# Optimization experiments

Measured on AMD Instinct MI355X. Metric: run time of the kernel, lower is better.

The kernel has to match this reference:

```python
import jax, jax.numpy as jnp
import numpy as np

N_QUBITS = 12
N_LAYERS = 4
BATCH = 1024


def _apply_1q(state, U, wire):
    # state: (B,) + (2,)*N complex; U: (2,2) shared or (B,2,2) batched.
    x = jnp.moveaxis(state, 1 + wire, 1)
    if U.ndim == 3:
        x = jnp.einsum('bij,bj...->bi...', U, x)
    else:
        x = jnp.einsum('ij,bj...->bi...', U, x)
    return jnp.moveaxis(x, 1, 1 + wire)


def _apply_cnot(state, c, t):
    # CNOT: flip target axis on the control=1 slice.
    x = jnp.moveaxis(state, (1 + c, 1 + t), (1, 2))
    x = x.at[:, 1].set(x[:, 1, ::-1])
    return jnp.moveaxis(x, (1, 2), (1 + c, 1 + t))


def _rot_matrices(w):
    # PennyLane Rot(phi, theta, omega) = RZ(omega) RY(theta) RZ(phi); w: (N, 3) -> (N, 2, 2)
    phi, theta, omega = w[:, 0], w[:, 1], w[:, 2]
    c = jnp.cos(theta / 2).astype(jnp.complex64)
    s = jnp.sin(theta / 2).astype(jnp.complex64)
    ep = jnp.exp(0.5j * (phi + omega).astype(jnp.complex64))  # e^{+i(phi+omega)/2}
    em = jnp.exp(0.5j * (phi - omega).astype(jnp.complex64))  # e^{+i(phi-omega)/2}
    m00 = jnp.conj(ep) * c
    m01 = -em * s
    m10 = jnp.conj(em) * s
    m11 = ep * c
    return jnp.stack([jnp.stack([m00, m01], -1), jnp.stack([m10, m11], -1)], -2)


def _circuit(x, weights):
    B = x.shape[0]
    n = N_QUBITS
    # |0...0> initial state, batched, shaped (B, 2, 2, ..., 2)
    state = jnp.zeros((B, 2 ** n), jnp.complex64).at[:, 0].set(1.0)
    state = state.reshape((B,) + (2,) * n)
    # Angle encoding: RY(pi * x_i) on wire i (batched gate matrices)
    half = jnp.pi * x / 2  # (B, n)
    c = jnp.cos(half).astype(jnp.complex64)
    s = jnp.sin(half).astype(jnp.complex64)
    ry = jnp.stack([jnp.stack([c, -s], -1), jnp.stack([s, c], -1)], -2)  # (B, n, 2, 2)
    for i in range(n):
        state = _apply_1q(state, ry[:, i], i)
    # CNOT ring
    for i in range(n):
        state = _apply_cnot(state, i, (i + 1) % n)
    # StronglyEntanglingLayers, default ranges r_l = (l % (n-1)) + 1
    for l in range(N_LAYERS):
        U = _rot_matrices(weights[l])
        for i in range(n):
            state = _apply_1q(state, U[i], i)
        r = l % (n - 1) + 1
        for i in range(n):
            state = _apply_cnot(state, i, (i + r) % n)
    # PauliZ expectations: <Z_i> = sum_k |psi_k|^2 * (-1)^{bit_i(k)}
    probs = (state.real ** 2 + state.imag ** 2).reshape(B, 2 ** n)
    ks = np.arange(2 ** n)
    bits = (ks[:, None] >> (n - 1 - np.arange(n))) & 1  # wire 0 = most significant axis
    signs = jnp.asarray(1.0 - 2.0 * bits, jnp.float32)  # (2^n, n)
    return probs @ signs  # (B, n)


def setup_inputs():
    key = jax.random.key(0)
    k1, k2 = jax.random.split(key)
    x = jax.random.uniform(k1, (BATCH, N_QUBITS), jnp.float32)
    weights = jax.random.uniform(k2, (N_LAYERS, N_QUBITS, 3), jnp.float32)
    return {"x": x, "weights": weights}


def reference(x, weights):
    return _circuit(x, weights)
```

## Files before the change

kernel.cpp:

```cpp
#include <hip/hip_runtime.h>

#define NQ 12
#define NLAYERS 4

typedef float v2f __attribute__((ext_vector_type(2)));
typedef unsigned uint2v __attribute__((ext_vector_type(2)));

template<int CTRL>
__device__ __forceinline__ float dppmov(float v) {
    return __uint_as_float((unsigned)__builtin_amdgcn_update_dpp(
        0, (int)__float_as_uint(v), CTRL, 0xF, 0xF, true));
}

template<int LB>
__device__ __forceinline__ float lx(float v, int lane) {
    if constexpr (LB == 0) {
        return dppmov<0xB1>(v);
    } else if constexpr (LB == 1) {
        return dppmov<0x4E>(v);
    } else if constexpr (LB == 2) {
        float a = dppmov<0x124>(v);
        float b = dppmov<0x12C>(v);
        return (lane & 4) ? a : b;
    } else if constexpr (LB == 3) {
        return dppmov<0x128>(v);
    } else if constexpr (LB == 4) {
#if __has_builtin(__builtin_amdgcn_permlane16_swap)
        uint2v r = __builtin_amdgcn_permlane16_swap(__float_as_uint(v), __float_as_uint(v), false, false);
        return __uint_as_float(r.x) + __uint_as_float(r.y) - v;
#else
        return __shfl_xor(v, 16, 64);
#endif
    } else {
#if __has_builtin(__builtin_amdgcn_permlane32_swap)
        uint2v r = __builtin_amdgcn_permlane32_swap(__float_as_uint(v), __float_as_uint(v), false, false);
        return __uint_as_float(r.x) + __uint_as_float(r.y) - v;
#else
        return __shfl_xor(v, 32, 64);
#endif
    }
}

template<int LB>
__device__ __forceinline__ v2f lxv(v2f a, int lane) {
    v2f r;
    r.x = lx<LB>(a.x, lane);
    r.y = lx<LB>(a.y, lane);
    return r;
}

__device__ __forceinline__ v2f swap2(v2f a) { return __builtin_shufflevector(a, a, 1, 0); }

template<int S>
__host__ __device__ constexpr int ringsrc_c(int k) {
    int s = k;
    for (int i = 11; i >= 0; --i) {
        const int pc = 11 - i;
        const int pt = 11 - ((i + S) % 12);
        s ^= ((s >> pc) & 1) << pt;
    }
    return s;
}

__host__ __device__ constexpr int ror1_4(int m) {
    return ((m >> 1) | ((m & 1) << 3)) & 15;
}
__host__ __device__ constexpr int phys_lin(int s) {
    return s ^ ror1_4((s >> 4) & 15);
}

struct LUT16 { int v[16]; };

template<int S>
__host__ __device__ constexpr LUT16 make_lr() {
    LUT16 a{};
    for (int r = 0; r < 16; ++r) a.v[r] = ringsrc_c<S>(r);
    return a;
}
template<int S>
__host__ __device__ constexpr LUT16 make_pr() {
    LUT16 a{};
    for (int r = 0; r < 16; ++r) a.v[r] = phys_lin(ringsrc_c<S>(r));
    return a;
}

template<int S>
__host__ __device__ constexpr bool grp_used(int h) {
    for (int r = 0; r < 16; ++r)
        if (((ringsrc_c<S>(r) >> 10) & 3) == h) return true;
    return false;
}


template<int RB>
__device__ __forceinline__ void gate_reg(v2f (&st)[16], const v2f* __restrict__ M) {
    const v2f m00xx = M[0], m00yy = M[1], m01xx = M[2], m01yy = M[3];
    const v2f m10xx = M[4], m10yy = M[5], m11xx = M[6], m11yy = M[7];
    #pragma unroll
    for (int r = 0; r < 16; ++r) if (!(r & (1 << RB))) {
        const int r1 = r | (1 << RB);
        v2f a0 = st[r], a1 = st[r1];
        st[r]  = m00xx * a0 + m00yy * swap2(a0) + m01xx * a1 + m01yy * swap2(a1);
        st[r1] = m10xx * a0 + m10yy * swap2(a0) + m11xx * a1 + m11yy * swap2(a1);
    }
}

template<int LB>
__device__ __forceinline__ void gate_lane(v2f (&st)[16], int lane, const v2f* __restrict__ M) {
    const bool hi = (lane >> LB) & 1;
    const v2f mSxx = hi ? M[6] : M[0], mSyy = hi ? M[7] : M[1];
    const v2f mOxx = hi ? M[4] : M[2], mOyy = hi ? M[5] : M[3];
    #pragma unroll
    for (int r = 0; r < 16; ++r) {
        v2f own = st[r];
        v2f oth = lxv<LB>(own, lane);
        st[r] = mSxx * own + mSyy * swap2(own) + mOxx * oth + mOyy * swap2(oth);
    }
}

template<int S, int H>
__device__ __forceinline__ void trip_group(v2f (&st)[16], int pb, int rowbase,
                                           const v2f* xch, const v2f* m4) {
    if constexpr (grp_used<S>(H)) {
        const int row = rowbase ^ H;
        v2f mxx[4], myy[4];
        #pragma unroll
        for (int j = 0; j < 4; ++j) {
            mxx[j] = m4[(row * 4 + j) * 2 + 0];
            myy[j] = m4[(row * 4 + j) * 2 + 1];
        }
        constexpr LUT16 LR = make_lr<S>();
        constexpr LUT16 PR = make_pr<S>();
        #pragma unroll
        for (int r = 0; r < 16; ++r) {
            if (((LR.v[r] >> 10) & 3) == H) {
                const int a = (pb ^ PR.v[r]) & 1023;
                v2f o0 = xch[a];
                v2f o1 = xch[a + 1024];
                v2f o2 = xch[a + 2048];
                v2f o3 = xch[a + 3072];
                st[r] = mxx[0] * o0 + myy[0] * swap2(o0)
                      + mxx[1] * o1 + myy[1] * swap2(o1)
                      + mxx[2] * o2 + myy[2] * swap2(o2)
                      + mxx[3] * o3 + myy[3] * swap2(o3);
            }
        }
    }
}

template<int S>
__device__ __forceinline__ void fused_trip(v2f (&st)[16], int wbase, int lsw,
                                           v2f* xch, const v2f* m4) {
    #pragma unroll
    for (int r = 0; r < 16; ++r) xch[wbase | (r ^ lsw)] = st[r];
    __syncthreads();
    const int sb = ringsrc_c<S>(wbase);
    const int pb = phys_lin(sb);
    const int rowbase = (sb >> 10) & 3;
    trip_group<S, 0>(st, pb, rowbase, xch, m4);
    trip_group<S, 1>(st, pb, rowbase, xch, m4);
    trip_group<S, 2>(st, pb, rowbase, xch, m4);
    trip_group<S, 3>(st, pb, rowbase, xch, m4);
    __syncthreads();
}

template<int S>
__device__ __forceinline__ void do_layer(v2f (&st)[16], int lane, int wbase, int lsw,
                                         v2f* xch, const v2f* m4,
                                         const v2f* __restrict__ Mw) {
    gate_lane<5>(st, lane, Mw + 2 * 8);
    gate_lane<4>(st, lane, Mw + 3 * 8);
    gate_lane<3>(st, lane, Mw + 4 * 8);
    gate_lane<2>(st, lane, Mw + 5 * 8);
    gate_lane<1>(st, lane, Mw + 6 * 8);
    gate_lane<0>(st, lane, Mw + 7 * 8);
    gate_reg<3>(st, Mw + 8 * 8);
    gate_reg<2>(st, Mw + 9 * 8);
    gate_reg<1>(st, Mw + 10 * 8);
    gate_reg<0>(st, Mw + 11 * 8);
    fused_trip<S>(st, wbase, lsw, xch, m4);
}

__global__ void prep_mats(const float* __restrict__ w3, v2f* __restrict__ mats) {
    int t = threadIdx.x;
    if (t < NLAYERS * NQ) {
        float phi = w3[t * 3 + 0], th = w3[t * 3 + 1], om = w3[t * 3 + 2];
        float ct = cosf(0.5f * th), s = sinf(0.5f * th);
        float ap = 0.5f * (phi + om), am = 0.5f * (phi - om);
        float cap = cosf(ap), sap = sinf(ap);
        float cam = cosf(am), sam = sinf(am);
        float2 m00 = make_float2( cap * ct, -sap * ct);
        float2 m01 = make_float2(-cam * s,  -sam * s);
        float2 m10 = make_float2( cam * s,  -sam * s);
        float2 m11 = make_float2( cap * ct,  sap * ct);
        v2f* M = mats + t * 8;
        M[0] = v2f{m00.x, m00.x};  M[1] = v2f{-m00.y, m00.y};
        M[2] = v2f{m01.x, m01.x};  M[3] = v2f{-m01.y, m01.y};
        M[4] = v2f{m10.x, m10.x};  M[5] = v2f{-m10.y, m10.y};
        M[6] = v2f{m11.x, m11.x};  M[7] = v2f{-m11.y, m11.y};
    }
    if (t < NLAYERS) {
        const int l = t;
        float2 mm[2][2][2];
        for (int w = 0; w < 2; ++w) {
            float phi = w3[(l * NQ + w) * 3 + 0], th = w3[(l * NQ + w) * 3 + 1],
                  om  = w3[(l * NQ + w) * 3 + 2];
            float ct = cosf(0.5f * th), s = sinf(0.5f * th);
            float ap = 0.5f * (phi + om), am = 0.5f * (phi - om);
            float cap = cosf(ap), sap = sinf(ap);
            float cam = cosf(am), sam = sinf(am);
            mm[w][0][0] = make_float2( cap * ct, -sap * ct);
            mm[w][0][1] = make_float2(-cam * s,  -sam * s);
            mm[w][1][0] = make_float2( cam * s,  -sam * s);
            mm[w][1][1] = make_float2( cap * ct,  sap * ct);
        }
        v2f* M4 = mats + NLAYERS * 96 + l * 32;
        for (int i = 0; i < 4; ++i)
            for (int j = 0; j < 4; ++j) {
                float2 a = mm[0][i >> 1][j >> 1];
                float2 bq = mm[1][i & 1][j & 1];
                float2 pq = make_float2(a.x * bq.x - a.y * bq.y, a.x * bq.y + a.y * bq.x);
                M4[(i * 4 + j) * 2 + 0] = v2f{pq.x, pq.x};
                M4[(i * 4 + j) * 2 + 1] = v2f{-pq.y, pq.y};
            }
    }
}

__device__ __forceinline__ float wsum(float v, int lane) {
    v += lx<5>(v, lane); v += lx<4>(v, lane); v += lx<3>(v, lane);
    v += lx<2>(v, lane); v += lx<1>(v, lane); v += lx<0>(v, lane);
    return v;
}

__global__ __launch_bounds__(256)
__attribute__((amdgpu_waves_per_eu(2, 4)))
void qsim_kernel(
    const float* __restrict__ x,
    const v2f* __restrict__ mats,
    float* __restrict__ out)
{
    __shared__ v2f xch[4096];
    __shared__ v2f m4l[NLAYERS * 32];

    const int b     = blockIdx.x;
    const int tid   = threadIdx.x;
    const int wv    = tid >> 6;
    const int lane  = tid & 63;
    const int wbase = (wv << 10) | (lane << 4);
    const int lsw   = ror1_4(lane & 15);

    if (tid < NLAYERS * 32) m4l[tid] = mats[NLAYERS * 96 + tid];

    const float PI = 3.14159265358979323846f;

    float cs[12], sn[12];
    #pragma unroll
    for (int w = 0; w < 12; ++w) {
        float h = 0.5f * PI * x[b * NQ + w];
        __sincosf(h, &sn[w], &cs[w]);
    }
    const int sbi = ringsrc_c<1>(wbase);
    float LF = 1.f;
    #pragma unroll
    for (int w = 2; w < 8; ++w)
        LF *= ((sbi >> (11 - w)) & 1) ? sn[w] : cs[w];
    constexpr LUT16 L1R = make_lr<1>();
    v2f st[16];
    #pragma unroll
    for (int r = 0; r < 16; ++r) {
        const int idx = sbi ^ L1R.v[r];
        float f = LF;
        f *= ((idx >> 11) & 1) ? sn[0]  : cs[0];
        f *= ((idx >> 10) & 1) ? sn[1]  : cs[1];
        f *= ((idx >> 3) & 1)  ? sn[8]  : cs[8];
        f *= ((idx >> 2) & 1)  ? sn[9]  : cs[9];
        f *= ((idx >> 1) & 1)  ? sn[10] : cs[10];
        f *= ( idx       & 1)  ? sn[11] : cs[11];
        st[r] = v2f{f, 0.f};
    }

    do_layer<1>(st, lane, wbase, lsw, xch, m4l + 0,   mats + 0);
    do_layer<2>(st, lane, wbase, lsw, xch, m4l + 32,  mats + 96);
    do_layer<3>(st, lane, wbase, lsw, xch, m4l + 64,  mats + 192);
    do_layer<4>(st, lane, wbase, lsw, xch, m4l + 96,  mats + 288);

    float S = 0.f;
    float aR[4] = {0.f, 0.f, 0.f, 0.f};
    #pragma unroll
    for (int r = 0; r < 16; ++r) {
        v2f sq = st[r] * st[r];
        float pr = sq.x + sq.y;
        S += pr;
        #pragma unroll
        for (int rb = 0; rb < 4; ++rb)
            aR[rb] += ((r >> rb) & 1) ? -pr : pr;
    }

    float* red = (float*)xch;

    {
        float T = wsum(S, lane);
        if (lane == 0) {
            red[wv * 12 + 0] = ((wv >> 1) & 1) ? -T : T;
            red[wv * 12 + 1] = (wv & 1) ? -T : T;
        }
    }
    #pragma unroll
    for (int W = 2; W < 8; ++W) {
        float v0 = ((lane >> (7 - W)) & 1) ? -S : S;
        v0 = wsum(v0, lane);
        if (lane == 0) red[wv * 12 + W] = v0;
    }
    #pragma unroll
    for (int W = 8; W < 12; ++W) {
        float v0 = wsum(aR[11 - W], lane);
        if (lane == 0) red[wv * 12 + W] = v0;
    }
    __syncthreads();
    if (tid < 12)
        out[b * NQ + tid] = red[tid] + red[12 + tid] + red[24 + tid] + red[36 + tid];
}

extern "C" void kernel_launch(void* const* d_in, const int* in_sizes, int n_in,
                              void* d_out, int out_size, void* d_ws, size_t ws_size,
                              hipStream_t stream) {
    const float* x  = (const float*)d_in[0];
    const float* w3 = (const float*)d_in[1];
    float* out = (float*)d_out;
    v2f* mats = (v2f*)d_ws;
    int batch = in_sizes[0] / NQ;
    prep_mats<<<1, 64, 0, stream>>>(w3, mats);
    qsim_kernel<<<batch, 256, 0, stream>>>(x, mats, out);
}
```

Measured before the change: 59.07 us.

## Process two batch items per block, interleaving gate compute with LDS exchange

Each block now simulates two batch elements, keeping two state register sets, and alternates so that the register-local gates of one state run while the other state's shared-memory exchange read is pending. The 4x4 exchange matrices are now read from global memory instead of being staged in LDS. The grid is halved and the waves_per_eu hint is relaxed. This aims to hide LDS latency and barrier stalls behind ALU work, at the cost of doubled register pressure, lower occupancy and more barriers per element pair.

```diff
diff --git a/kernel.cpp b/kernel.cpp
--- a/kernel.cpp
+++ b/kernel.cpp
@@ -83,7 +83,6 @@
     for (int r = 0; r < 16; ++r) a.v[r] = phys_lin(ringsrc_c<S>(r));
     return a;
 }
-
 template<int S>
 __host__ __device__ constexpr bool grp_used(int h) {
     for (int r = 0; r < 16; ++r)
@@ -118,16 +117,34 @@
     }
 }
 
+__device__ __forceinline__ void do_gates(v2f (&st)[16], int lane, const v2f* __restrict__ Mw) {
+    gate_lane<5>(st, lane, Mw + 2 * 8);
+    gate_lane<4>(st, lane, Mw + 3 * 8);
+    gate_lane<3>(st, lane, Mw + 4 * 8);
+    gate_lane<2>(st, lane, Mw + 5 * 8);
+    gate_lane<1>(st, lane, Mw + 6 * 8);
+    gate_lane<0>(st, lane, Mw + 7 * 8);
+    gate_reg<3>(st, Mw + 8 * 8);
+    gate_reg<2>(st, Mw + 9 * 8);
+    gate_reg<1>(st, Mw + 10 * 8);
+    gate_reg<0>(st, Mw + 11 * 8);
+}
+
+__device__ __forceinline__ void trip_write(const v2f (&st)[16], int wbase, int lsw, v2f* xch) {
+    #pragma unroll
+    for (int r = 0; r < 16; ++r) xch[wbase | (r ^ lsw)] = st[r];
+}
+
 template<int S, int H>
 __device__ __forceinline__ void trip_group(v2f (&st)[16], int pb, int rowbase,
-                                           const v2f* xch, const v2f* m4) {
+                                           const v2f* xch, const v2f* __restrict__ m4g) {
     if constexpr (grp_used<S>(H)) {
         const int row = rowbase ^ H;
         v2f mxx[4], myy[4];
         #pragma unroll
         for (int j = 0; j < 4; ++j) {
-            mxx[j] = m4[(row * 4 + j) * 2 + 0];
-            myy[j] = m4[(row * 4 + j) * 2 + 1];
+            mxx[j] = m4g[(row * 4 + j) * 2 + 0];
+            myy[j] = m4g[(row * 4 + j) * 2 + 1];
         }
         constexpr LUT16 LR = make_lr<S>();
         constexpr LUT16 PR = make_pr<S>();
@@ -149,36 +166,15 @@
 }
 
 template<int S>
-__device__ __forceinline__ void fused_trip(v2f (&st)[16], int wbase, int lsw,
-                                           v2f* xch, const v2f* m4) {
-    #pragma unroll
-    for (int r = 0; r < 16; ++r) xch[wbase | (r ^ lsw)] = st[r];
-    __syncthreads();
+__device__ __forceinline__ void trip_read(v2f (&st)[16], int wbase,
+                                          const v2f* xch, const v2f* __restrict__ m4g) {
     const int sb = ringsrc_c<S>(wbase);
     const int pb = phys_lin(sb);
     const int rowbase = (sb >> 10) & 3;
-    trip_group<S, 0>(st, pb, rowbase, xch, m4);
-    trip_group<S, 1>(st, pb, rowbase, xch, m4);
-    trip_group<S, 2>(st, pb, rowbase, xch, m4);
-    trip_group<S, 3>(st, pb, rowbase, xch, m4);
-    __syncthreads();
-}
-
-template<int S>
-__device__ __forceinline__ void do_layer(v2f (&st)[16], int lane, int wbase, int lsw,
-                                         v2f* xch, const v2f* m4,
-                                         const v2f* __restrict__ Mw) {
-    gate_lane<5>(st, lane, Mw + 2 * 8);
-    gate_lane<4>(st, lane, Mw + 3 * 8);
-    gate_lane<3>(st, lane, Mw + 4 * 8);
-    gate_lane<2>(st, lane, Mw + 5 * 8);
-    gate_lane<1>(st, lane, Mw + 6 * 8);
-    gate_lane<0>(st, lane, Mw + 7 * 8);
-    gate_reg<3>(st, Mw + 8 * 8);
-    gate_reg<2>(st, Mw + 9 * 8);
-    gate_reg<1>(st, Mw + 10 * 8);
-    gate_reg<0>(st, Mw + 11 * 8);
-    fused_trip<S>(st, wbase, lsw, xch, m4);
+    trip_group<S, 0>(st, pb, rowbase, xch, m4g);
+    trip_group<S, 1>(st, pb, rowbase, xch, m4g);
+    trip_group<S, 2>(st, pb, rowbase, xch, m4g);
+    trip_group<S, 3>(st, pb, rowbase, xch, m4g);
 }
 
 __global__ void prep_mats(const float* __restrict__ w3, v2f* __restrict__ mats) {
@@ -232,31 +228,13 @@
     return v;
 }
 
-__global__ __launch_bounds__(256)
-__attribute__((amdgpu_waves_per_eu(2, 4)))
-void qsim_kernel(
-    const float* __restrict__ x,
-    const v2f* __restrict__ mats,
-    float* __restrict__ out)
-{
-    __shared__ v2f xch[4096];
-    __shared__ v2f m4l[NLAYERS * 32];
-
-    const int b     = blockIdx.x;
-    const int tid   = threadIdx.x;
-    const int wv    = tid >> 6;
-    const int lane  = tid & 63;
-    const int wbase = (wv << 10) | (lane << 4);
-    const int lsw   = ror1_4(lane & 15);
-
-    if (tid < NLAYERS * 32) m4l[tid] = mats[NLAYERS * 96 + tid];
-
+__device__ __forceinline__ void init_state(v2f (&st)[16], const float* __restrict__ xb,
+                                           int wbase) {
     const float PI = 3.14159265358979323846f;
-
     float cs[12], sn[12];
     #pragma unroll
     for (int w = 0; w < 12; ++w) {
-        float h = 0.5f * PI * x[b * NQ + w];
+        float h = 0.5f * PI * xb[w];
         __sincosf(h, &sn[w], &cs[w]);
     }
     const int sbi = ringsrc_c<1>(wbase);
@@ -265,7 +243,6 @@
     for (int w = 2; w < 8; ++w)
         LF *= ((sbi >> (11 - w)) & 1) ? sn[w] : cs[w];
     constexpr LUT16 L1R = make_lr<1>();
-    v2f st[16];
     #pragma unroll
     for (int r = 0; r < 16; ++r) {
         const int idx = sbi ^ L1R.v[r];
@@ -278,12 +255,10 @@
         f *= ( idx       & 1)  ? sn[11] : cs[11];
         st[r] = v2f{f, 0.f};
     }
-
-    do_layer<1>(st, lane, wbase, lsw, xch, m4l + 0,   mats + 0);
-    do_layer<2>(st, lane, wbase, lsw, xch, m4l + 32,  mats + 96);
-    do_layer<3>(st, lane, wbase, lsw, xch, m4l + 64,  mats + 192);
-    do_layer<4>(st, lane, wbase, lsw, xch, m4l + 96,  mats + 288);
-
+}
+
+__device__ __forceinline__ void epi_vals(const v2f (&st)[16], int lane, int wv,
+                                         float (&v)[12]) {
     float S = 0.f;
     float aR[4] = {0.f, 0.f, 0.f, 0.f};
     #pragma unroll
@@ -295,30 +270,84 @@
         for (int rb = 0; rb < 4; ++rb)
             aR[rb] += ((r >> rb) & 1) ? -pr : pr;
     }
-
-    float* red = (float*)xch;
-
-    {
-        float T = wsum(S, lane);
-        if (lane == 0) {
-            red[wv * 12 + 0] = ((wv >> 1) & 1) ? -T : T;
-            red[wv * 12 + 1] = (wv & 1) ? -T : T;
-        }
-    }
+    float T = wsum(S, lane);
+    v[0] = ((wv >> 1) & 1) ? -T : T;
+    v[1] = (wv & 1) ? -T : T;
     #pragma unroll
     for (int W = 2; W < 8; ++W) {
         float v0 = ((lane >> (7 - W)) & 1) ? -S : S;
-        v0 = wsum(v0, lane);
-        if (lane == 0) red[wv * 12 + W] = v0;
-    }
-    #pragma unroll
-    for (int W = 8; W < 12; ++W) {
-        float v0 = wsum(aR[11 - W], lane);
-        if (lane == 0) red[wv * 12 + W] = v0;
-    }
+        v[W] = wsum(v0, lane);
+    }
+    #pragma unroll
+    for (int W = 8; W < 12; ++W)
+        v[W] = wsum(aR[11 - W], lane);
+}
+
+__global__ __launch_bounds__(256)
+__attribute__((amdgpu_waves_per_eu(2)))
+void qsim_kernel(
+    const float* __restrict__ x,
+    const v2f* __restrict__ mats,
+    float* __restrict__ out)
+{
+    __shared__ v2f xch[4096];
+
+    const int bA    = 2 * blockIdx.x;
+    const int bB    = bA + 1;
+    const int tid   = threadIdx.x;
+    const int wv    = tid >> 6;
+    const int lane  = tid & 63;
+    const int wbase = (wv << 10) | (lane << 4);
+    const int lsw   = ror1_4(lane & 15);
+
+    v2f stA[16], stB[16];
+    init_state(stA, x + bA * NQ, wbase);
+    init_state(stB, x + bB * NQ, wbase);
+
+    const v2f* M0 = mats + 0;
+    const v2f* M1 = mats + 96;
+    const v2f* M2 = mats + 192;
+    const v2f* M3 = mats + 288;
+    const v2f* m4 = mats + NLAYERS * 96;
+
+    do_gates(stA, lane, M0);
+    trip_write(stA, wbase, lsw, xch); __syncthreads();
+    do_gates(stB, lane, M0);  trip_read<1>(stA, wbase, xch, m4 + 0);  __syncthreads();
+    trip_write(stB, wbase, lsw, xch); __syncthreads();
+    do_gates(stA, lane, M1);  trip_read<1>(stB, wbase, xch, m4 + 0);  __syncthreads();
+    trip_write(stA, wbase, lsw, xch); __syncthreads();
+    do_gates(stB, lane, M1);  trip_read<2>(stA, wbase, xch, m4 + 32); __syncthreads();
+    trip_write(stB, wbase, lsw, xch); __syncthreads();
+    do_gates(stA, lane, M2);  trip_read<2>(stB, wbase, xch, m4 + 32); __syncthreads();
+    trip_write(stA, wbase, lsw, xch); __syncthreads();
+    do_gates(stB, lane, M2);  trip_read<3>(stA, wbase, xch, m4 + 64); __syncthreads();
+    trip_write(stB, wbase, lsw, xch); __syncthreads();
+    do_gates(stA, lane, M3);  trip_read<3>(stB, wbase, xch, m4 + 64); __syncthreads();
+    trip_write(stA, wbase, lsw, xch); __syncthreads();
+    do_gates(stB, lane, M3);  trip_read<4>(stA, wbase, xch, m4 + 96); __syncthreads();
+    trip_write(stB, wbase, lsw, xch); __syncthreads();
+
+    float vA[12];
+    epi_vals(stA, lane, wv, vA);
+    trip_read<4>(stB, wbase, xch, m4 + 96);
     __syncthreads();
-    if (tid < 12)
-        out[b * NQ + tid] = red[tid] + red[12 + tid] + red[24 + tid] + red[36 + tid];
+
+    float vB[12];
+    epi_vals(stB, lane, wv, vB);
+
+    float* red = (float*)xch;
+    if (lane == 0) {
+        #pragma unroll
+        for (int q = 0; q < 12; ++q) {
+            red[wv * 12 + q]      = vA[q];
+            red[48 + wv * 12 + q] = vB[q];
+        }
+    }
+    __syncthreads();
+    if (tid < 12) {
+        out[bA * NQ + tid] = red[tid] + red[12 + tid] + red[24 + tid] + red[36 + tid];
+        out[bB * NQ + tid] = red[48 + tid] + red[60 + tid] + red[72 + tid] + red[84 + tid];
+    }
 }
 
 extern "C" void kernel_launch(void* const* d_in, const int* in_sizes, int n_in,
@@ -330,5 +359,5 @@
     v2f* mats = (v2f*)d_ws;
     int batch = in_sizes[0] / NQ;
     prep_mats<<<1, 64, 0, stream>>>(w3, mats);
-    qsim_kernel<<<batch, 256, 0, stream>>>(x, mats, out);
-}
+    qsim_kernel<<<batch / 2, 256, 0, stream>>>(x, mats, out);
+}
```

New measurement: 69.21 us. +17.2%, slower.

## Double-buffer LDS exchange to drop per-layer trailing barrier, read 4x4 mats from global

Applied to the files above, without the earlier changes.

Alternates two LDS exchange buffers across layers so the trailing __syncthreads after each exchange read can be removed, leaving one barrier per layer. The 4x4 two-qubit matrices are now read straight from global memory instead of being staged in LDS. The waves_per_eu upper bound is relaxed. LDS use doubles to 64KB, which may cut blocks per CU, and the matrix loads now go through the global/scalar cache path.

```diff
diff --git a/kernel.cpp b/kernel.cpp
--- a/kernel.cpp
+++ b/kernel.cpp
@@ -83,7 +83,6 @@
     for (int r = 0; r < 16; ++r) a.v[r] = phys_lin(ringsrc_c<S>(r));
     return a;
 }
-
 template<int S>
 __host__ __device__ constexpr bool grp_used(int h) {
     for (int r = 0; r < 16; ++r)
@@ -118,56 +117,7 @@
     }
 }
 
-template<int S, int H>
-__device__ __forceinline__ void trip_group(v2f (&st)[16], int pb, int rowbase,
-                                           const v2f* xch, const v2f* m4) {
-    if constexpr (grp_used<S>(H)) {
-        const int row = rowbase ^ H;
-        v2f mxx[4], myy[4];
-        #pragma unroll
-        for (int j = 0; j < 4; ++j) {
-            mxx[j] = m4[(row * 4 + j) * 2 + 0];
-            myy[j] = m4[(row * 4 + j) * 2 + 1];
-        }
-        constexpr LUT16 LR = make_lr<S>();
-        constexpr LUT16 PR = make_pr<S>();
-        #pragma unroll
-        for (int r = 0; r < 16; ++r) {
-            if (((LR.v[r] >> 10) & 3) == H) {
-                const int a = (pb ^ PR.v[r]) & 1023;
-                v2f o0 = xch[a];
-                v2f o1 = xch[a + 1024];
-                v2f o2 = xch[a + 2048];
-                v2f o3 = xch[a + 3072];
-                st[r] = mxx[0] * o0 + myy[0] * swap2(o0)
-                      + mxx[1] * o1 + myy[1] * swap2(o1)
-                      + mxx[2] * o2 + myy[2] * swap2(o2)
-                      + mxx[3] * o3 + myy[3] * swap2(o3);
-            }
-        }
-    }
-}
-
-template<int S>
-__device__ __forceinline__ void fused_trip(v2f (&st)[16], int wbase, int lsw,
-                                           v2f* xch, const v2f* m4) {
-    #pragma unroll
-    for (int r = 0; r < 16; ++r) xch[wbase | (r ^ lsw)] = st[r];
-    __syncthreads();
-    const int sb = ringsrc_c<S>(wbase);
-    const int pb = phys_lin(sb);
-    const int rowbase = (sb >> 10) & 3;
-    trip_group<S, 0>(st, pb, rowbase, xch, m4);
-    trip_group<S, 1>(st, pb, rowbase, xch, m4);
-    trip_group<S, 2>(st, pb, rowbase, xch, m4);
-    trip_group<S, 3>(st, pb, rowbase, xch, m4);
-    __syncthreads();
-}
-
-template<int S>
-__device__ __forceinline__ void do_layer(v2f (&st)[16], int lane, int wbase, int lsw,
-                                         v2f* xch, const v2f* m4,
-                                         const v2f* __restrict__ Mw) {
+__device__ __forceinline__ void do_gates(v2f (&st)[16], int lane, const v2f* __restrict__ Mw) {
     gate_lane<5>(st, lane, Mw + 2 * 8);
     gate_lane<4>(st, lane, Mw + 3 * 8);
     gate_lane<3>(st, lane, Mw + 4 * 8);
@@ -178,7 +128,53 @@
     gate_reg<2>(st, Mw + 9 * 8);
     gate_reg<1>(st, Mw + 10 * 8);
     gate_reg<0>(st, Mw + 11 * 8);
-    fused_trip<S>(st, wbase, lsw, xch, m4);
+}
+
+__device__ __forceinline__ void trip_write(const v2f (&st)[16], int wbase, int lsw, v2f* buf) {
+    #pragma unroll
+    for (int r = 0; r < 16; ++r) buf[wbase | (r ^ lsw)] = st[r];
+}
+
+template<int S, int H>
+__device__ __forceinline__ void trip_group(v2f (&st)[16], int pb, int rowbase,
+                                           const v2f* buf, const v2f* __restrict__ m4g) {
+    if constexpr (grp_used<S>(H)) {
+        const int row = rowbase ^ H;
+        v2f mxx[4], myy[4];
+        #pragma unroll
+        for (int j = 0; j < 4; ++j) {
+            mxx[j] = m4g[(row * 4 + j) * 2 + 0];
+            myy[j] = m4g[(row * 4 + j) * 2 + 1];
+        }
+        constexpr LUT16 LR = make_lr<S>();
+        constexpr LUT16 PR = make_pr<S>();
+        #pragma unroll
+        for (int r = 0; r < 16; ++r) {
+            if (((LR.v[r] >> 10) & 3) == H) {
+                const int a = (pb ^ PR.v[r]) & 1023;
+                v2f o0 = buf[a];
+                v2f o1 = buf[a + 1024];
+                v2f o2 = buf[a + 2048];
+                v2f o3 = buf[a + 3072];
+                st[r] = mxx[0] * o0 + myy[0] * swap2(o0)
+                      + mxx[1] * o1 + myy[1] * swap2(o1)
+                      + mxx[2] * o2 + myy[2] * swap2(o2)
+                      + mxx[3] * o3 + myy[3] * swap2(o3);
+            }
+        }
+    }
+}
+
+template<int S>
+__device__ __forceinline__ void trip_read(v2f (&st)[16], int wbase,
+                                          const v2f* buf, const v2f* __restrict__ m4g) {
+    const int sb = ringsrc_c<S>(wbase);
+    const int pb = phys_lin(sb);
+    const int rowbase = (sb >> 10) & 3;
+    trip_group<S, 0>(st, pb, rowbase, buf, m4g);
+    trip_group<S, 1>(st, pb, rowbase, buf, m4g);
+    trip_group<S, 2>(st, pb, rowbase, buf, m4g);
+    trip_group<S, 3>(st, pb, rowbase, buf, m4g);
 }
 
 __global__ void prep_mats(const float* __restrict__ w3, v2f* __restrict__ mats) {
@@ -233,14 +229,14 @@
 }
 
 __global__ __launch_bounds__(256)
-__attribute__((amdgpu_waves_per_eu(2, 4)))
+__attribute__((amdgpu_waves_per_eu(2)))
 void qsim_kernel(
     const float* __restrict__ x,
     const v2f* __restrict__ mats,
     float* __restrict__ out)
 {
-    __shared__ v2f xch[4096];
-    __shared__ v2f m4l[NLAYERS * 32];
+    __shared__ v2f xchA[4096];
+    __shared__ v2f xchB[4096];
 
     const int b     = blockIdx.x;
     const int tid   = threadIdx.x;
@@ -248,8 +244,6 @@
     const int lane  = tid & 63;
     const int wbase = (wv << 10) | (lane << 4);
     const int lsw   = ror1_4(lane & 15);
-
-    if (tid < NLAYERS * 32) m4l[tid] = mats[NLAYERS * 96 + tid];
 
     const float PI = 3.14159265358979323846f;
 
@@ -279,10 +273,23 @@
         st[r] = v2f{f, 0.f};
     }
 
-    do_layer<1>(st, lane, wbase, lsw, xch, m4l + 0,   mats + 0);
-    do_layer<2>(st, lane, wbase, lsw, xch, m4l + 32,  mats + 96);
-    do_layer<3>(st, lane, wbase, lsw, xch, m4l + 64,  mats + 192);
-    do_layer<4>(st, lane, wbase, lsw, xch, m4l + 96,  mats + 288);
+    const v2f* m4 = mats + NLAYERS * 96;
+
+    do_gates(st, lane, mats + 0);
+    trip_write(st, wbase, lsw, xchA);  __syncthreads();
+    trip_read<1>(st, wbase, xchA, m4 + 0);
+
+    do_gates(st, lane, mats + 96);
+    trip_write(st, wbase, lsw, xchB);  __syncthreads();
+    trip_read<2>(st, wbase, xchB, m4 + 32);
+
+    do_gates(st, lane, mats + 192);
+    trip_write(st, wbase, lsw, xchA);  __syncthreads();
+    trip_read<3>(st, wbase, xchA, m4 + 64);
+
+    do_gates(st, lane, mats + 288);
+    trip_write(st, wbase, lsw, xchB);  __syncthreads();
+    trip_read<4>(st, wbase, xchB, m4 + 96);
 
     float S = 0.f;
     float aR[4] = {0.f, 0.f, 0.f, 0.f};
@@ -296,7 +303,8 @@
             aR[rb] += ((r >> rb) & 1) ? -pr : pr;
     }
 
-    float* red = (float*)xch;
+    __syncthreads();
+    float* red = (float*)xchA;
 
     {
         float T = wsum(S, lane);
```

Measured after the change: 60.65 us. 1.03x slower.

## Decompose Rot gates into real RY plus batched diagonal phase factors

Applied to the files above, without the earlier changes.

Each Rot gate is split into its RZ phases and a real RY rotation. All RZ phases in a layer are merged into one diagonal phase multiply per register, built incrementally from precomputed cos/sin factors. The final layer's trailing RZ phases are dropped because they do not change the PauliZ expectations. The lane and register gates now do real-scalar rotations instead of full complex 2x2 products, and the two-wire shared-memory step uses a real 4x4 matrix with an optional phase. This cuts per-gate arithmetic and matrix-register pressure, at the cost of extra sincos and phase-product work per layer. It also loosens the waves_per_eu upper bound.

```diff
diff --git a/kernel.cpp b/kernel.cpp
--- a/kernel.cpp
+++ b/kernel.cpp
@@ -49,8 +49,6 @@
     return r;
 }
 
-__device__ __forceinline__ v2f swap2(v2f a) { return __builtin_shufflevector(a, a, 1, 0); }
-
 template<int S>
 __host__ __device__ constexpr int ringsrc_c(int k) {
     int s = k;
@@ -83,7 +81,6 @@
     for (int r = 0; r < 16; ++r) a.v[r] = phys_lin(ringsrc_c<S>(r));
     return a;
 }
-
 template<int S>
 __host__ __device__ constexpr bool grp_used(int h) {
     for (int r = 0; r < 16; ++r)
@@ -91,138 +88,162 @@
     return false;
 }
 
-
 template<int RB>
-__device__ __forceinline__ void gate_reg(v2f (&st)[16], const v2f* __restrict__ M) {
-    const v2f m00xx = M[0], m00yy = M[1], m01xx = M[2], m01yy = M[3];
-    const v2f m10xx = M[4], m10yy = M[5], m11xx = M[6], m11yy = M[7];
+__device__ __forceinline__ void ry_reg(v2f (&st)[16], float c, float s) {
     #pragma unroll
     for (int r = 0; r < 16; ++r) if (!(r & (1 << RB))) {
         const int r1 = r | (1 << RB);
         v2f a0 = st[r], a1 = st[r1];
-        st[r]  = m00xx * a0 + m00yy * swap2(a0) + m01xx * a1 + m01yy * swap2(a1);
-        st[r1] = m10xx * a0 + m10yy * swap2(a0) + m11xx * a1 + m11yy * swap2(a1);
-    }
-}
-
+        st[r]  = c * a0 - s * a1;
+        st[r1] = s * a0 + c * a1;
+    }
+}
 template<int LB>
-__device__ __forceinline__ void gate_lane(v2f (&st)[16], int lane, const v2f* __restrict__ M) {
-    const bool hi = (lane >> LB) & 1;
-    const v2f mSxx = hi ? M[6] : M[0], mSyy = hi ? M[7] : M[1];
-    const v2f mOxx = hi ? M[4] : M[2], mOyy = hi ? M[5] : M[3];
+__device__ __forceinline__ void ry_lane(v2f (&st)[16], int lane, float c, float s) {
+    const float so = ((lane >> LB) & 1) ? s : -s;
     #pragma unroll
     for (int r = 0; r < 16; ++r) {
-        v2f own = st[r];
-        v2f oth = lxv<LB>(own, lane);
-        st[r] = mSxx * own + mSyy * swap2(own) + mOxx * oth + mOyy * swap2(oth);
-    }
-}
-
-template<int S, int H>
+        v2f oth = lxv<LB>(st[r], lane);
+        st[r] = c * st[r] + so * oth;
+    }
+}
+
+__device__ __forceinline__ void diag_apply(v2f (&st)[16], float A, const float* __restrict__ f) {
+    float sA, cA;
+    __sincosf(A, &sA, &cA);
+    v2f p[16];
+    p[0] = v2f{cA, sA};
+    #pragma unroll
+    for (int r = 1; r < 16; ++r) {
+        const int b = (r & 1) ? 0 : ((r & 2) ? 1 : ((r & 4) ? 2 : 3));
+        const v2f q = p[r & (r - 1)];
+        const float fc = f[2 * b], fs = f[2 * b + 1];
+        p[r] = v2f{fc * q.x - fs * q.y, fc * q.y + fs * q.x};
+    }
+    #pragma unroll
+    for (int r = 0; r < 16; ++r) {
+        const v2f a = st[r], q = p[r];
+        st[r] = v2f{a.x * q.x - a.y * q.y, a.x * q.y + a.y * q.x};
+    }
+}
+
+__device__ __forceinline__ void trip_write(const v2f (&st)[16], int wbase, int lsw, v2f* buf) {
+    #pragma unroll
+    for (int r = 0; r < 16; ++r) buf[wbase | (r ^ lsw)] = st[r];
+}
+
+template<int S, int H, bool RP>
 __device__ __forceinline__ void trip_group(v2f (&st)[16], int pb, int rowbase,
-                                           const v2f* xch, const v2f* m4) {
+                                           const v2f* buf, const float* __restrict__ P) {
     if constexpr (grp_used<S>(H)) {
         const int row = rowbase ^ H;
-        v2f mxx[4], myy[4];
-        #pragma unroll
-        for (int j = 0; j < 4; ++j) {
-            mxx[j] = m4[(row * 4 + j) * 2 + 0];
-            myy[j] = m4[(row * 4 + j) * 2 + 1];
-        }
+        const float rm0 = P[66 + row * 4 + 0], rm1 = P[66 + row * 4 + 1],
+                    rm2 = P[66 + row * 4 + 2], rm3 = P[66 + row * 4 + 3];
+        float pc = 0.f, ps = 0.f;
+        if constexpr (RP) { pc = P[82 + 2 * row]; ps = P[83 + 2 * row]; }
         constexpr LUT16 LR = make_lr<S>();
         constexpr LUT16 PR = make_pr<S>();
         #pragma unroll
         for (int r = 0; r < 16; ++r) {
             if (((LR.v[r] >> 10) & 3) == H) {
                 const int a = (pb ^ PR.v[r]) & 1023;
-                v2f o0 = xch[a];
-                v2f o1 = xch[a + 1024];
-                v2f o2 = xch[a + 2048];
-                v2f o3 = xch[a + 3072];
-                st[r] = mxx[0] * o0 + myy[0] * swap2(o0)
-                      + mxx[1] * o1 + myy[1] * swap2(o1)
-                      + mxx[2] * o2 + myy[2] * swap2(o2)
-                      + mxx[3] * o3 + myy[3] * swap2(o3);
+                v2f acc = rm0 * buf[a]
+                        + rm1 * buf[a + 1024]
+                        + rm2 * buf[a + 2048]
+                        + rm3 * buf[a + 3072];
+                if constexpr (RP)
+                    st[r] = v2f{acc.x * pc - acc.y * ps, acc.y * pc + acc.x * ps};
+                else
+                    st[r] = acc;
             }
         }
     }
 }
 
-template<int S>
-__device__ __forceinline__ void fused_trip(v2f (&st)[16], int wbase, int lsw,
-                                           v2f* xch, const v2f* m4) {
-    #pragma unroll
-    for (int r = 0; r < 16; ++r) xch[wbase | (r ^ lsw)] = st[r];
-    __syncthreads();
+template<int S, bool RP>
+__device__ __forceinline__ void trip_read(v2f (&st)[16], int wbase,
+                                          const v2f* buf, const float* __restrict__ P) {
     const int sb = ringsrc_c<S>(wbase);
     const int pb = phys_lin(sb);
     const int rowbase = (sb >> 10) & 3;
-    trip_group<S, 0>(st, pb, rowbase, xch, m4);
-    trip_group<S, 1>(st, pb, rowbase, xch, m4);
-    trip_group<S, 2>(st, pb, rowbase, xch, m4);
-    trip_group<S, 3>(st, pb, rowbase, xch, m4);
+    trip_group<S, 0, RP>(st, pb, rowbase, buf, P);
+    trip_group<S, 1, RP>(st, pb, rowbase, buf, P);
+    trip_group<S, 2, RP>(st, pb, rowbase, buf, P);
+    trip_group<S, 3, RP>(st, pb, rowbase, buf, P);
+}
+
+template<int S, bool FULL>
+__device__ __forceinline__ void do_layer(v2f (&st)[16], int lane, int wv, int wbase, int lsw,
+                                         v2f* xch, const float* __restrict__ P) {
+    {
+        float A = P[64];
+        A += ((wv >> 1) & 1) ? 2.f * P[24 + 0] : 0.f;
+        A += (wv & 1)        ? 2.f * P[24 + 1] : 0.f;
+        #pragma unroll
+        for (int w = 2; w < 8; ++w)
+            A += ((lane >> (7 - w)) & 1) ? 2.f * P[24 + w] : 0.f;
+        diag_apply(st, A, P + 48);
+    }
+    ry_lane<5>(st, lane, P[2],  P[14]);
+    ry_lane<4>(st, lane, P[3],  P[15]);
+    ry_lane<3>(st, lane, P[4],  P[16]);
+    ry_lane<2>(st, lane, P[5],  P[17]);
+    ry_lane<1>(st, lane, P[6],  P[18]);
+    ry_lane<0>(st, lane, P[7],  P[19]);
+    ry_reg<3>(st, P[8],  P[20]);
+    ry_reg<2>(st, P[9],  P[21]);
+    ry_reg<1>(st, P[10], P[22]);
+    ry_reg<0>(st, P[11], P[23]);
+    if constexpr (FULL) {
+        float A = P[65];
+        #pragma unroll
+        for (int w = 2; w < 8; ++w)
+            A += ((lane >> (7 - w)) & 1) ? 2.f * P[36 + w] : 0.f;
+        diag_apply(st, A, P + 56);
+    }
+    trip_write(st, wbase, lsw, xch);
     __syncthreads();
-}
-
-template<int S>
-__device__ __forceinline__ void do_layer(v2f (&st)[16], int lane, int wbase, int lsw,
-                                         v2f* xch, const v2f* m4,
-                                         const v2f* __restrict__ Mw) {
-    gate_lane<5>(st, lane, Mw + 2 * 8);
-    gate_lane<4>(st, lane, Mw + 3 * 8);
-    gate_lane<3>(st, lane, Mw + 4 * 8);
-    gate_lane<2>(st, lane, Mw + 5 * 8);
-    gate_lane<1>(st, lane, Mw + 6 * 8);
-    gate_lane<0>(st, lane, Mw + 7 * 8);
-    gate_reg<3>(st, Mw + 8 * 8);
-    gate_reg<2>(st, Mw + 9 * 8);
-    gate_reg<1>(st, Mw + 10 * 8);
-    gate_reg<0>(st, Mw + 11 * 8);
-    fused_trip<S>(st, wbase, lsw, xch, m4);
-}
-
-__global__ void prep_mats(const float* __restrict__ w3, v2f* __restrict__ mats) {
+    trip_read<S, FULL>(st, wbase, xch, P);
+    __syncthreads();
+}
+
+__global__ void prep_mats(const float* __restrict__ w3, float* __restrict__ prm) {
     int t = threadIdx.x;
     if (t < NLAYERS * NQ) {
+        int l = t / 12, w = t % 12;
         float phi = w3[t * 3 + 0], th = w3[t * 3 + 1], om = w3[t * 3 + 2];
-        float ct = cosf(0.5f * th), s = sinf(0.5f * th);
-        float ap = 0.5f * (phi + om), am = 0.5f * (phi - om);
-        float cap = cosf(ap), sap = sinf(ap);
-        float cam = cosf(am), sam = sinf(am);
-        float2 m00 = make_float2( cap * ct, -sap * ct);
-        float2 m01 = make_float2(-cam * s,  -sam * s);
-        float2 m10 = make_float2( cam * s,  -sam * s);
-        float2 m11 = make_float2( cap * ct,  sap * ct);
-        v2f* M = mats + t * 8;
-        M[0] = v2f{m00.x, m00.x};  M[1] = v2f{-m00.y, m00.y};
-        M[2] = v2f{m01.x, m01.x};  M[3] = v2f{-m01.y, m01.y};
-        M[4] = v2f{m10.x, m10.x};  M[5] = v2f{-m10.y, m10.y};
-        M[6] = v2f{m11.x, m11.x};  M[7] = v2f{-m11.y, m11.y};
+        float* P = prm + l * 128;
+        P[w]      = cosf(0.5f * th);
+        P[12 + w] = sinf(0.5f * th);
+        P[24 + w] = 0.5f * phi;
+        P[36 + w] = 0.5f * om;
     }
     if (t < NLAYERS) {
         const int l = t;
-        float2 mm[2][2][2];
-        for (int w = 0; w < 2; ++w) {
-            float phi = w3[(l * NQ + w) * 3 + 0], th = w3[(l * NQ + w) * 3 + 1],
-                  om  = w3[(l * NQ + w) * 3 + 2];
-            float ct = cosf(0.5f * th), s = sinf(0.5f * th);
-            float ap = 0.5f * (phi + om), am = 0.5f * (phi - om);
-            float cap = cosf(ap), sap = sinf(ap);
-            float cam = cosf(am), sam = sinf(am);
-            mm[w][0][0] = make_float2( cap * ct, -sap * ct);
-            mm[w][0][1] = make_float2(-cam * s,  -sam * s);
-            mm[w][1][0] = make_float2( cam * s,  -sam * s);
-            mm[w][1][1] = make_float2( cap * ct,  sap * ct);
+        const float* W = w3 + l * 36;
+        float* P = prm + l * 128;
+        float nphi = 0.f, nomg = 0.f;
+        for (int w = 0; w < 12; ++w) nphi -= 0.5f * W[w * 3 + 0];
+        for (int w = 2; w < 12; ++w) nomg -= 0.5f * W[w * 3 + 2];
+        P[64] = nphi;
+        P[65] = nomg;
+        for (int b = 0; b < 4; ++b) {
+            int w = 11 - b;
+            P[48 + 2 * b] = cosf(W[w * 3 + 0]);  P[49 + 2 * b] = sinf(W[w * 3 + 0]);
+            P[56 + 2 * b] = cosf(W[w * 3 + 2]);  P[57 + 2 * b] = sinf(W[w * 3 + 2]);
         }
-        v2f* M4 = mats + NLAYERS * 96 + l * 32;
-        for (int i = 0; i < 4; ++i)
-            for (int j = 0; j < 4; ++j) {
-                float2 a = mm[0][i >> 1][j >> 1];
-                float2 bq = mm[1][i & 1][j & 1];
-                float2 pq = make_float2(a.x * bq.x - a.y * bq.y, a.x * bq.y + a.y * bq.x);
-                M4[(i * 4 + j) * 2 + 0] = v2f{pq.x, pq.x};
-                M4[(i * 4 + j) * 2 + 1] = v2f{-pq.y, pq.y};
-            }
+        float c0 = cosf(0.5f * W[0 * 3 + 1]), s0 = sinf(0.5f * W[0 * 3 + 1]);
+        float c1 = cosf(0.5f * W[1 * 3 + 1]), s1 = sinf(0.5f * W[1 * 3 + 1]);
+        float R0[2][2] = {{c0, -s0}, {s0, c0}};
+        float R1[2][2] = {{c1, -s1}, {s1, c1}};
+        float ho0 = 0.5f * W[0 * 3 + 2], ho1 = 0.5f * W[1 * 3 + 2];
+        for (int i = 0; i < 4; ++i) {
+            for (int j = 0; j < 4; ++j)
+                P[66 + i * 4 + j] = R0[i >> 1][j >> 1] * R1[i & 1][j & 1];
+            float beta = (2 * (i >> 1) - 1) * ho0 + (2 * (i & 1) - 1) * ho1;
+            P[82 + 2 * i] = cosf(beta);
+            P[83 + 2 * i] = sinf(beta);
+        }
     }
 }
 
@@ -233,14 +254,13 @@
 }
 
 __global__ __launch_bounds__(256)
-__attribute__((amdgpu_waves_per_eu(2, 4)))
+__attribute__((amdgpu_waves_per_eu(2)))
 void qsim_kernel(
     const float* __restrict__ x,
-    const v2f* __restrict__ mats,
+    const float* __restrict__ prm,
     float* __restrict__ out)
 {
     __shared__ v2f xch[4096];
-    __shared__ v2f m4l[NLAYERS * 32];
 
     const int b     = blockIdx.x;
     const int tid   = threadIdx.x;
@@ -248,8 +268,6 @@
     const int lane  = tid & 63;
     const int wbase = (wv << 10) | (lane << 4);
     const int lsw   = ror1_4(lane & 15);
-
-    if (tid < NLAYERS * 32) m4l[tid] = mats[NLAYERS * 96 + tid];
 
     const float PI = 3.14159265358979323846f;
 
@@ -279,10 +297,10 @@
         st[r] = v2f{f, 0.f};
     }
 
-    do_layer<1>(st, lane, wbase, lsw, xch, m4l + 0,   mats + 0);
-    do_layer<2>(st, lane, wbase, lsw, xch, m4l + 32,  mats + 96);
-    do_layer<3>(st, lane, wbase, lsw, xch, m4l + 64,  mats + 192);
-    do_layer<4>(st, lane, wbase, lsw, xch, m4l + 96,  mats + 288);
+    do_layer<1, true >(st, lane, wv, wbase, lsw, xch, prm + 0);
+    do_layer<2, true >(st, lane, wv, wbase, lsw, xch, prm + 128);
+    do_layer<3, true >(st, lane, wv, wbase, lsw, xch, prm + 256);
+    do_layer<4, false>(st, lane, wv, wbase, lsw, xch, prm + 384);
 
     float S = 0.f;
     float aR[4] = {0.f, 0.f, 0.f, 0.f};
@@ -327,8 +345,8 @@
     const float* x  = (const float*)d_in[0];
     const float* w3 = (const float*)d_in[1];
     float* out = (float*)d_out;
-    v2f* mats = (v2f*)d_ws;
+    float* prm = (float*)d_ws;
     int batch = in_sizes[0] / NQ;
-    prep_mats<<<1, 64, 0, stream>>>(w3, mats);
-    qsim_kernel<<<batch, 256, 0, stream>>>(x, mats, out);
-}
+    prep_mats<<<1, 64, 0, stream>>>(w3, prm);
+    qsim_kernel<<<batch, 256, 0, stream>>>(x, prm, out);
+}
```

Result: slower. 61.77 us (+4.6%).
